# Kernel optimization log

Hardware: AMD Instinct MI355X
Metric: run time of the kernel (lower is better)

Reference implementation:

```python
import jax, jax.numpy as jnp
import numpy as np
from jax import lax

B, T, D, H, O, L = 128, 2048, 64, 128, 32, 2


def _rnn_layer(x, lengths, W_ih, W_hh, b_ih, b_hh):
    """One tanh RNN layer over padded [B,T,*] input with packed semantics:
    hidden state is frozen at steps t >= lengths[b] (those steps do not exist
    in the packed sequence). Returns per-step hidden states [B,T,H]."""
    Bl, Tl, _ = x.shape
    Hl = W_hh.shape[0]
    # precompute input projection once: [B,T,H]
    x_proj = jnp.einsum('btd,hd->bth', x, W_ih) + b_ih + b_hh

    def step(h, inp):
        xp, t = inp  # xp: [B,H], t: scalar
        h_new = jnp.tanh(xp + h @ W_hh.T)
        h = jnp.where((t < lengths)[:, None], h_new, h)
        return h, h

    h0 = jnp.zeros((Bl, Hl), dtype=x.dtype)
    _, ys = lax.scan(step, h0, (x_proj.transpose(1, 0, 2), jnp.arange(Tl)))
    return ys.transpose(1, 0, 2)  # [B,T,H]


def setup_inputs() -> dict:
    key = jax.random.key(0)
    ks = jax.random.split(key, 12)
    x = jax.random.normal(ks[0], (B, T, D), dtype=jnp.float32)
    # descending-sorted lengths in [1, T] (pack_padded_sequence enforce_sorted)
    lengths = jnp.sort(jax.random.randint(ks[1], (B,), 1, T + 1).astype(jnp.int32))[::-1]
    s_in = 1.0 / np.sqrt(H)
    W_ih0 = jax.random.uniform(ks[2], (H, D), minval=-s_in, maxval=s_in)
    W_hh0 = jax.random.uniform(ks[3], (H, H), minval=-s_in, maxval=s_in)
    b_ih0 = jax.random.uniform(ks[4], (H,), minval=-s_in, maxval=s_in)
    b_hh0 = jax.random.uniform(ks[5], (H,), minval=-s_in, maxval=s_in)
    W_ih1 = jax.random.uniform(ks[6], (H, H), minval=-s_in, maxval=s_in)
    W_hh1 = jax.random.uniform(ks[7], (H, H), minval=-s_in, maxval=s_in)
    b_ih1 = jax.random.uniform(ks[8], (H,), minval=-s_in, maxval=s_in)
    b_hh1 = jax.random.uniform(ks[9], (H,), minval=-s_in, maxval=s_in)
    W_fc = jax.random.uniform(ks[10], (O, H), minval=-s_in, maxval=s_in)
    b_fc = jax.random.uniform(ks[11], (O,), minval=-s_in, maxval=s_in)
    return {"x": x, "lengths": lengths,
            "W_ih0": W_ih0, "W_hh0": W_hh0, "b_ih0": b_ih0, "b_hh0": b_hh0,
            "W_ih1": W_ih1, "W_hh1": W_hh1, "b_ih1": b_ih1, "b_hh1": b_hh1,
            "W_fc": W_fc, "b_fc": b_fc}


def reference(x, lengths, W_ih0, W_hh0, b_ih0, b_hh0,
              W_ih1, W_hh1, b_ih1, b_hh1, W_fc, b_fc):
    h1 = _rnn_layer(x, lengths, W_ih0, W_hh0, b_ih0, b_hh0)   # [B,T,H]
    h2 = _rnn_layer(h1, lengths, W_ih1, W_hh1, b_ih1, b_hh1)  # [B,T,H]
    # pad_packed_sequence zero-fills positions t >= length
    mask = (jnp.arange(T)[None, :] < lengths[:, None])[..., None]
    out = jnp.where(mask, h2, 0.0)
    # fc is applied to the zero-padded tensor (padded rows become b_fc)
    return jnp.einsum('bth,oh->bto', out, W_fc) + b_fc
```

## Files before the change

### kernel.cpp

```cpp
#include <hip/hip_runtime.h>

#define BB 128
#define TT 2048
#define DD 64
#define HH 128
#define OO 32
#define NB 16
#define SCALE 2.885390081777927f

typedef _Float16 f16x8 __attribute__((ext_vector_type(8)));
typedef __fp16   pk16x2 __attribute__((ext_vector_type(2)));
typedef float    f32x4 __attribute__((ext_vector_type(4)));

#define MFMA16(a,b,c) __builtin_amdgcn_mfma_f32_16x16x32_f16((a),(b),(c),0,0,0)

__device__ __forceinline__ f32x4 load4(const float* p){ return *(const f32x4*)p; }

union U8 { uint2 u[2]; f16x8 v; };

__device__ __forceinline__ f16x8 afrag_s(const float* p, float s){
    float4 a = *(const float4*)p, b = *(const float4*)(p+4);
    f16x8 r;
    r[0]=(_Float16)(a.x*s); r[1]=(_Float16)(a.y*s); r[2]=(_Float16)(a.z*s); r[3]=(_Float16)(a.w*s);
    r[4]=(_Float16)(b.x*s); r[5]=(_Float16)(b.y*s); r[6]=(_Float16)(b.z*s); r[7]=(_Float16)(b.w*s);
    return r;
}

__device__ __forceinline__ float tanh_pre(float z){
#if __has_builtin(__builtin_amdgcn_exp2f)
    float e = __builtin_amdgcn_exp2f(z);
#else
    float e = exp2f(z);
#endif
    return __builtin_fmaf(-2.f, __builtin_amdgcn_rcpf(1.f + e), 1.f);
}

__device__ __forceinline__ unsigned pk2(float a, float b){
    union { pk16x2 h; unsigned u; } c;
    c.h = __builtin_amdgcn_cvt_pkrtz(a, b);
    return c.u;
}

#define XSTR 72
extern "C" __global__ void __launch_bounds__(256)
proj_kernel(const float* __restrict__ x, const float* __restrict__ W_ih0,
            const float* __restrict__ b_ih0, const float* __restrict__ b_hh0,
            _Float16* __restrict__ xp0)
{
    const int tid = threadIdx.x;
    const int w = tid >> 6, lane = tid & 63;
    const int n = lane & 15, q = lane >> 4;
    const size_t row0 = (size_t)blockIdx.x * 64;

    __shared__ __align__(16) _Float16 XT[64][XSTR];

    #pragma unroll
    for (int it = 0; it < 4; ++it){
        float4 v = *(const float4*)(x + row0*DD + it*1024 + tid*4);
        int rr = it*16 + (tid >> 4), d0 = (tid & 15)*4;
        union { uint2 u; _Float16 h[4]; } c;
        c.h[0]=(_Float16)v.x; c.h[1]=(_Float16)v.y; c.h[2]=(_Float16)v.z; c.h[3]=(_Float16)v.w;
        *(uint2*)&XT[rr][d0] = c.u;
    }

    f16x8 A[8][2]; f32x4 bv[8];
    #pragma unroll
    for (int mt = 0; mt < 8; ++mt){
        #pragma unroll
        for (int kt = 0; kt < 2; ++kt)
            A[mt][kt] = afrag_s(W_ih0 + (mt*16 + n)*DD + kt*32 + q*8, SCALE);
        bv[mt] = (load4(b_ih0 + mt*16 + q*4) + load4(b_hh0 + mt*16 + q*4)) * SCALE;
    }
    __syncthreads();

    const _Float16* xr = &XT[w*16 + n][0];
    f16x8 B0 = *(const f16x8*)(xr + q*8);
    f16x8 B1 = *(const f16x8*)(xr + 32 + q*8);

    _Float16* orow = xp0 + (row0 + w*16 + n)*HH + q*4;
    #pragma unroll
    for (int mt = 0; mt < 8; ++mt){
        f32x4 acc = bv[mt];
        acc = MFMA16(A[mt][0], B0, acc);
        acc = MFMA16(A[mt][1], B1, acc);
        union { uint2 u; _Float16 h[4]; } s;
        #pragma unroll
        for (int r = 0; r < 4; ++r) s.h[r] = (_Float16)acc[r];
        *(uint2*)(orow + mt*16) = s.u;
    }
}

extern "C" __global__ void __launch_bounds__(256)
fill_kernel(const int* __restrict__ lengths, const float* __restrict__ b_fc,
            float* __restrict__ out)
{
    size_t idx = (size_t)blockIdx.x*256 + threadIdx.x;
    #pragma unroll
    for (int k = 0; k < 4; ++k, idx += (size_t)2048*256){
        int o4 = (int)(idx & 7);
        int t  = (int)((idx >> 3) & 2047);
        int b  = (int)(idx >> 14);
        if (t >= lengths[b])
            ((float4*)out)[idx] = *(const float4*)(b_fc + o4*4);
    }
}

#define LSTR2 132
#define PHB   (NB*LSTR2*2)

#define STEP_L1(T_, P_, XS_) do {                                             \
    const int t_ = (T_);                                                      \
    U8 bh1[4];                                                                \
    _Pragma("unroll")                                                         \
    for (int kt = 0; kt < 4; ++kt){                                           \
        bh1[kt].u[0] = *(const uint2*)(h1b + (P_)*PHB + kt*64);               \
        bh1[kt].u[1] = *(const uint2*)(h1b + (P_)*PHB + kt*64 + 8);           \
    }                                                                         \
    f32x4 z[4];                                                               \
    const bool doZ0 = (t_ < maxlen);                                          \
    if (doZ0){                                                                \
        _Pragma("unroll")                                                     \
        for (int m = 0; m < 4; ++m){                                          \
            union { uint2 u; _Float16 h[4]; } c; c.u = XS_[m];                \
            _Pragma("unroll")                                                 \
            for (int r = 0; r < 4; ++r) z[m][r] = (float)c.h[r];              \
        }                                                                     \
        _Pragma("unroll")                                                     \
        for (int kt = 0; kt < 4; ++kt)                                        \
            _Pragma("unroll")                                                 \
            for (int m = 0; m < 4; ++m)                                       \
                z[m] = MFMA16(A0[m][kt], bh1[kt].v, z[m]);                    \
    }                                                                         \
    {             \
        const int tl = (t_ + 2 < TT) ? (t_ + 2) : (TT - 1);                   \
        _Pragma("unroll")                                                     \
        for (int m = 0; m < 4; ++m)                                           \
            XS_[m] = *(const uint2*)(xpb + (size_t)tl*256 + m*32);            \
    }                                                                         \
    if (doZ0){                                                                \
        _Pragma("unroll")                                                     \
        for (int m = 0; m < 4; ++m){                                          \
            uint2 v;                                                          \
            v.x = pk2(tanh_pre(z[m][0]), tanh_pre(z[m][1]));                  \
            v.y = pk2(tanh_pre(z[m][2]), tanh_pre(z[m][3]));                  \
            *(uint2*)((char*)H1T + ((P_)^1)*PHB + n*264 + (w*4+m)*32 + q*8) = v; \
        }                                                                     \
    }                                                                         \
    asm volatile("s_waitcnt lgkmcnt(0)\n\ts_barrier" ::: "memory");           \
} while (0)

#define STEP_L2(T_, P_) do {                                                  \
    const int t_ = (T_);                                                      \
    U8 bh1[4], bh2[4];                                                        \
    _Pragma("unroll")                                                         \
    for (int kt = 0; kt < 4; ++kt){                                           \
        bh1[kt].u[0] = *(const uint2*)(h1b + (P_)*PHB + kt*64);               \
        bh1[kt].u[1] = *(const uint2*)(h1b + (P_)*PHB + kt*64 + 8);           \
        bh2[kt].u[0] = *(const uint2*)(h2b + (P_)*PHB + kt*64);               \
        bh2[kt].u[1] = *(const uint2*)(h2b + (P_)*PHB + kt*64 + 8);           \
    }                                                                         \
    const bool doZ1 = (t_ >= 1) && (t_ <= maxlen);                            \
    f32x4 z[4];                                                               \
    if (doZ1){                                                                \
        f32x4 y[4];                                                           \
        _Pragma("unroll")                                                     \
        for (int m = 0; m < 4; ++m){                                          \
            z[m] = b1v[m];                                                    \
            y[m][0]=0.f; y[m][1]=0.f; y[m][2]=0.f; y[m][3]=0.f;               \
        }                                                                     \
        _Pragma("unroll")                                                     \
        for (int kt = 0; kt < 4; ++kt)                                        \
            _Pragma("unroll")                                                 \
            for (int m = 0; m < 4; ++m){                                      \
                z[m] = MFMA16(Ai[m][kt], bh1[kt].v, z[m]);                    \
                y[m] = MFMA16(Ah[m][kt], bh2[kt].v, y[m]);                    \
            }                                                                 \
        _Pragma("unroll")                                                     \
        for (int m = 0; m < 4; ++m) z[m] += y[m];                             \
    }                                                                         \
    if (t_ >= 2){                                                             \
        f32x4 zf = bfv;                                                       \
        _Pragma("unroll")                                                     \
        for (int kt = 0; kt < 4; ++kt) zf = MFMA16(Af[kt], bh2[kt].v, zf);    \
        if (t_ - 2 < lenn){                                                   \
            float4 sv; sv.x=zf[0]; sv.y=zf[1]; sv.z=zf[2]; sv.w=zf[3];        \
            *(float4*)(obase + (size_t)(t_-2)*OO) = sv;                       \
        }                                                                     \
    }                                                                         \
    if (doZ1){                                                                \
        _Pragma("unroll")                                                     \
        for (int m = 0; m < 4; ++m){                                          \
            uint2 v;                                                          \
            v.x = pk2(tanh_pre(z[m][0]), tanh_pre(z[m][1]));                  \
            v.y = pk2(tanh_pre(z[m][2]), tanh_pre(z[m][3]));                  \
            *(uint2*)((char*)H2T + ((P_)^1)*PHB + n*264 + (wl*4+m)*32 + q*8) = v; \
        }                                                                     \
    }                                                                         \
    asm volatile("s_waitcnt lgkmcnt(0)\n\ts_barrier" ::: "memory");           \
} while (0)

extern "C" __global__ void __launch_bounds__(256, 1)
scan_kernel(const _Float16* __restrict__ xp0, const int* __restrict__ lengths,
            const float* __restrict__ W_hh0,
            const float* __restrict__ W_ih1, const float* __restrict__ W_hh1,
            const float* __restrict__ b_ih1, const float* __restrict__ b_hh1,
            const float* __restrict__ W_fc,  const float* __restrict__ b_fc,
            float* __restrict__ out)
{
    const int tid  = threadIdx.x;
    const int w    = tid >> 6, lane = tid & 63;
    const int n    = lane & 15, q = lane >> 4;
    const int rbase= blockIdx.x * NB;

    __shared__ __align__(16) _Float16 H1T[2][NB][LSTR2];
    __shared__ __align__(16) _Float16 H2T[2][NB][LSTR2];

    for (int idx = tid; idx < (2*NB*LSTR2)/2; idx += 256){
        ((unsigned*)H1T)[idx] = 0u;
        ((unsigned*)H2T)[idx] = 0u;
    }

    const int lenn = lengths[rbase + n];
    int mx = lenn;
    #pragma unroll
    for (int s = 1; s < 16; s <<= 1){ int o = __shfl_xor(mx, s, 64); mx = max(mx, o); }
    const int maxlen = __builtin_amdgcn_readfirstlane(mx);

    const char* h1b = (const char*)H1T + n*264 + q*16;
    const char* h2b = (const char*)H2T + n*264 + q*16;

    __syncthreads();

    if (w < 2){
        f16x8 A0[4][4];
        #pragma unroll
        for (int m = 0; m < 4; ++m){
            const int row = (w*4 + m)*16 + n;
            #pragma unroll
            for (int kt = 0; kt < 4; ++kt)
                A0[m][kt] = afrag_s(W_hh0 + row*HH + kt*32 + q*8, SCALE);
        }
        const char* xpb = (const char*)(xp0 + ((size_t)(rbase+n)*TT)*HH)
                          + (w*4)*32 + q*8;

        uint2 xe[4], xo[4];
        #pragma unroll
        for (int m = 0; m < 4; ++m){
            xe[m] = *(const uint2*)(xpb + m*32);
            xo[m] = *(const uint2*)(xpb + 256 + m*32);
        }

        for (int t0 = 0; t0 <= maxlen + 1; t0 += 2){
            STEP_L1(t0,     0, xe);
            STEP_L1(t0 + 1, 1, xo);
        }
    } else {
        const int wl = w - 2, f = w & 1;
        f16x8 Ai[4][4], Ah[4][4];
        f32x4 b1v[4];
        #pragma unroll
        for (int m = 0; m < 4; ++m){
            const int row = (wl*4 + m)*16 + n;
            #pragma unroll
            for (int kt = 0; kt < 4; ++kt){
                Ai[m][kt] = afrag_s(W_ih1 + row*HH + kt*32 + q*8, SCALE);
                Ah[m][kt] = afrag_s(W_hh1 + row*HH + kt*32 + q*8, SCALE);
            }
            b1v[m] = (load4(b_ih1 + (wl*4+m)*16 + q*4)
                    + load4(b_hh1 + (wl*4+m)*16 + q*4)) * SCALE;
        }
        f16x8 Af[4];
        #pragma unroll
        for (int kt = 0; kt < 4; ++kt)
            Af[kt] = afrag_s(W_fc + (f*16 + n)*HH + kt*32 + q*8, 1.0f);
        const f32x4 bfv = load4(b_fc + f*16 + q*4);

        float* obase = out + ((size_t)(rbase+n)*TT)*OO + f*16 + q*4;

        for (int t0 = 0; t0 <= maxlen + 1; t0 += 2){
            STEP_L2(t0,     0);
            STEP_L2(t0 + 1, 1);
        }
    }
}

extern "C" void kernel_launch(void* const* d_in, const int* in_sizes, int n_in,
                              void* d_out, int out_size, void* d_ws, size_t ws_size,
                              hipStream_t stream)
{
    const float* x       = (const float*)d_in[0];
    const int*   lengths = (const int*)  d_in[1];
    const float* W_ih0   = (const float*)d_in[2];
    const float* W_hh0   = (const float*)d_in[3];
    const float* b_ih0   = (const float*)d_in[4];
    const float* b_hh0   = (const float*)d_in[5];
    const float* W_ih1   = (const float*)d_in[6];
    const float* W_hh1   = (const float*)d_in[7];
    const float* b_ih1   = (const float*)d_in[8];
    const float* b_hh1   = (const float*)d_in[9];
    const float* W_fc    = (const float*)d_in[10];
    const float* b_fc    = (const float*)d_in[11];

    _Float16* xp = (_Float16*)d_ws;

    proj_kernel<<<BB*TT/64, 256, 0, stream>>>(x, W_ih0, b_ih0, b_hh0, xp);
    fill_kernel<<<2048, 256, 0, stream>>>(lengths, b_fc, (float*)d_out);
    scan_kernel<<<BB/NB, 256, 0, stream>>>(xp, lengths, W_hh0,
                                           W_ih1, W_hh1, b_ih1, b_hh1,
                                           W_fc, b_fc, (float*)d_out);
}
```

Before: 1.631 ms.

## Fuse input projection and padding fill into the scan kernel

Removes the separate projection kernel and fp16 workspace. Layer-1 waves now read raw fp32 x each step and compute the W_ih0 projection with two extra MFMAs per output tile inside the recurrence. The bias fill for padded timesteps moves to the end of the scan kernel. This saves two launches and a round trip through global memory, but it adds MFMA work and wider fp32 loads on the serial critical path, and the fill now runs on only 8 blocks.

```diff
diff --git a/kernel.cpp b/kernel.cpp
--- a/kernel.cpp
+++ b/kernel.cpp
@@ -41,68 +41,11 @@
     return c.u;
 }
 
-#define XSTR 72
-extern "C" __global__ void __launch_bounds__(256)
-proj_kernel(const float* __restrict__ x, const float* __restrict__ W_ih0,
-            const float* __restrict__ b_ih0, const float* __restrict__ b_hh0,
-            _Float16* __restrict__ xp0)
-{
-    const int tid = threadIdx.x;
-    const int w = tid >> 6, lane = tid & 63;
-    const int n = lane & 15, q = lane >> 4;
-    const size_t row0 = (size_t)blockIdx.x * 64;
-
-    __shared__ __align__(16) _Float16 XT[64][XSTR];
-
-    #pragma unroll
-    for (int it = 0; it < 4; ++it){
-        float4 v = *(const float4*)(x + row0*DD + it*1024 + tid*4);
-        int rr = it*16 + (tid >> 4), d0 = (tid & 15)*4;
-        union { uint2 u; _Float16 h[4]; } c;
-        c.h[0]=(_Float16)v.x; c.h[1]=(_Float16)v.y; c.h[2]=(_Float16)v.z; c.h[3]=(_Float16)v.w;
-        *(uint2*)&XT[rr][d0] = c.u;
-    }
-
-    f16x8 A[8][2]; f32x4 bv[8];
-    #pragma unroll
-    for (int mt = 0; mt < 8; ++mt){
-        #pragma unroll
-        for (int kt = 0; kt < 2; ++kt)
-            A[mt][kt] = afrag_s(W_ih0 + (mt*16 + n)*DD + kt*32 + q*8, SCALE);
-        bv[mt] = (load4(b_ih0 + mt*16 + q*4) + load4(b_hh0 + mt*16 + q*4)) * SCALE;
-    }
-    __syncthreads();
-
-    const _Float16* xr = &XT[w*16 + n][0];
-    f16x8 B0 = *(const f16x8*)(xr + q*8);
-    f16x8 B1 = *(const f16x8*)(xr + 32 + q*8);
-
-    _Float16* orow = xp0 + (row0 + w*16 + n)*HH + q*4;
-    #pragma unroll
-    for (int mt = 0; mt < 8; ++mt){
-        f32x4 acc = bv[mt];
-        acc = MFMA16(A[mt][0], B0, acc);
-        acc = MFMA16(A[mt][1], B1, acc);
-        union { uint2 u; _Float16 h[4]; } s;
-        #pragma unroll
-        for (int r = 0; r < 4; ++r) s.h[r] = (_Float16)acc[r];
-        *(uint2*)(orow + mt*16) = s.u;
-    }
-}
-
-extern "C" __global__ void __launch_bounds__(256)
-fill_kernel(const int* __restrict__ lengths, const float* __restrict__ b_fc,
-            float* __restrict__ out)
-{
-    size_t idx = (size_t)blockIdx.x*256 + threadIdx.x;
-    #pragma unroll
-    for (int k = 0; k < 4; ++k, idx += (size_t)2048*256){
-        int o4 = (int)(idx & 7);
-        int t  = (int)((idx >> 3) & 2047);
-        int b  = (int)(idx >> 14);
-        if (t >= lengths[b])
-            ((float4*)out)[idx] = *(const float4*)(b_fc + o4*4);
-    }
+__device__ __forceinline__ f16x8 xfrag(float4 a, float4 b){
+    union { unsigned u[4]; f16x8 v; } c;
+    c.u[0] = pk2(a.x, a.y); c.u[1] = pk2(a.z, a.w);
+    c.u[2] = pk2(b.x, b.y); c.u[3] = pk2(b.z, b.w);
+    return c.v;
 }
 
 #define LSTR2 132
@@ -119,11 +62,13 @@
     f32x4 z[4];                                                               \
     const bool doZ0 = (t_ < maxlen);                                          \
     if (doZ0){                                                                \
-        _Pragma("unroll")                                                     \
-        for (int m = 0; m < 4; ++m){                                          \
-            union { uint2 u; _Float16 h[4]; } c; c.u = XS_[m];                \
-            _Pragma("unroll")                                                 \
-            for (int r = 0; r < 4; ++r) z[m][r] = (float)c.h[r];              \
+        f16x8 xB0 = xfrag(XS_[0], XS_[1]);                                    \
+        f16x8 xB1 = xfrag(XS_[2], XS_[3]);                                    \
+        _Pragma("unroll")                                                     \
+        for (int m = 0; m < 4; ++m){                                          \
+            z[m] = bv0[m];                                                    \
+            z[m] = MFMA16(Aih[m][0], xB0, z[m]);                              \
+            z[m] = MFMA16(Aih[m][1], xB1, z[m]);                              \
         }                                                                     \
         _Pragma("unroll")                                                     \
         for (int kt = 0; kt < 4; ++kt)                                        \
@@ -131,11 +76,13 @@
             for (int m = 0; m < 4; ++m)                                       \
                 z[m] = MFMA16(A0[m][kt], bh1[kt].v, z[m]);                    \
     }                                                                         \
-    {             \
+    {           \
         const int tl = (t_ + 2 < TT) ? (t_ + 2) : (TT - 1);                   \
-        _Pragma("unroll")                                                     \
-        for (int m = 0; m < 4; ++m)                                           \
-            XS_[m] = *(const uint2*)(xpb + (size_t)tl*256 + m*32);            \
+        const float* xq = xb + (size_t)tl*DD;                                 \
+        XS_[0] = *(const float4*)(xq);                                        \
+        XS_[1] = *(const float4*)(xq + 4);                                    \
+        XS_[2] = *(const float4*)(xq + 32);                                   \
+        XS_[3] = *(const float4*)(xq + 36);                                   \
     }                                                                         \
     if (doZ0){                                                                \
         _Pragma("unroll")                                                     \
@@ -200,8 +147,9 @@
 } while (0)
 
 extern "C" __global__ void __launch_bounds__(256, 1)
-scan_kernel(const _Float16* __restrict__ xp0, const int* __restrict__ lengths,
-            const float* __restrict__ W_hh0,
+scan_kernel(const float* __restrict__ x, const int* __restrict__ lengths,
+            const float* __restrict__ W_ih0, const float* __restrict__ W_hh0,
+            const float* __restrict__ b_ih0, const float* __restrict__ b_hh0,
             const float* __restrict__ W_ih1, const float* __restrict__ W_hh1,
             const float* __restrict__ b_ih1, const float* __restrict__ b_hh1,
             const float* __restrict__ W_fc,  const float* __restrict__ b_fc,
@@ -232,22 +180,31 @@
     __syncthreads();
 
     if (w < 2){
-        f16x8 A0[4][4];
+        f16x8 A0[4][4], Aih[4][2];
+        f32x4 bv0[4];
         #pragma unroll
         for (int m = 0; m < 4; ++m){
             const int row = (w*4 + m)*16 + n;
             #pragma unroll
             for (int kt = 0; kt < 4; ++kt)
                 A0[m][kt] = afrag_s(W_hh0 + row*HH + kt*32 + q*8, SCALE);
-        }
-        const char* xpb = (const char*)(xp0 + ((size_t)(rbase+n)*TT)*HH)
-                          + (w*4)*32 + q*8;
-
-        uint2 xe[4], xo[4];
-        #pragma unroll
-        for (int m = 0; m < 4; ++m){
-            xe[m] = *(const uint2*)(xpb + m*32);
-            xo[m] = *(const uint2*)(xpb + 256 + m*32);
+            #pragma unroll
+            for (int kt = 0; kt < 2; ++kt)
+                Aih[m][kt] = afrag_s(W_ih0 + row*DD + kt*32 + q*8, SCALE);
+            bv0[m] = (load4(b_ih0 + (w*4+m)*16 + q*4)
+                    + load4(b_hh0 + (w*4+m)*16 + q*4)) * SCALE;
+        }
+
+        const float* xb = x + ((size_t)(rbase+n)*TT)*DD + q*8;
+
+        float4 xe[4], xo[4];
+        {
+            const float* x0 = xb;
+            const float* x1 = xb + DD;
+            xe[0] = *(const float4*)(x0);      xe[1] = *(const float4*)(x0 + 4);
+            xe[2] = *(const float4*)(x0 + 32); xe[3] = *(const float4*)(x0 + 36);
+            xo[0] = *(const float4*)(x1);      xo[1] = *(const float4*)(x1 + 4);
+            xo[2] = *(const float4*)(x1 + 32); xo[3] = *(const float4*)(x1 + 36);
         }
 
         for (int t0 = 0; t0 <= maxlen + 1; t0 += 2){
@@ -281,6 +238,18 @@
             STEP_L2(t0,     0);
             STEP_L2(t0 + 1, 1);
         }
+    }
+
+    {
+        const int rl   = lane >> 4;
+        const int row  = w*4 + rl;
+        const int lr   = lengths[rbase + row];
+        const int o4   = lane & 7;
+        const int tpar = (lane >> 3) & 1;
+        const float4 bf4 = *(const float4*)(b_fc + o4*4);
+        float* ob = out + ((size_t)(rbase+row)*TT)*OO + o4*4;
+        for (int t = lr + tpar; t < TT; t += 2)
+            *(float4*)(ob + (size_t)t*OO) = bf4;
     }
 }
 
@@ -301,11 +270,8 @@
     const float* W_fc    = (const float*)d_in[10];
     const float* b_fc    = (const float*)d_in[11];
 
-    _Float16* xp = (_Float16*)d_ws;
-
-    proj_kernel<<<BB*TT/64, 256, 0, stream>>>(x, W_ih0, b_ih0, b_hh0, xp);
-    fill_kernel<<<2048, 256, 0, stream>>>(lengths, b_fc, (float*)d_out);
-    scan_kernel<<<BB/NB, 256, 0, stream>>>(xp, lengths, W_hh0,
+    scan_kernel<<<BB/NB, 256, 0, stream>>>(x, lengths, W_ih0, W_hh0,
+                                           b_ih0, b_hh0,
                                            W_ih1, W_hh1, b_ih1, b_hh1,
                                            W_fc, b_fc, (float*)d_out);
 }
```

Result: slower. 1.674 ms (+2.6%).
